# Performance work log

Measured on AMD Instinct MI355X. Metric: run time of the kernel, lower is better.

Reference implementation:

```python
import jax, jax.numpy as jnp
import numpy as np

B, N, D_IN, D_OUT = 8, 2048, 64, 64


def setup_inputs() -> dict:
    key = jax.random.key(0)
    k1, k2, k3, k4 = jax.random.split(key, 4)
    x = jax.random.normal(k1, (B, N, D_IN), dtype=jnp.float32)
    adj_matrix = jax.random.randint(k2, (B, N, N), 0, 2, dtype=jnp.int32)
    W = jax.random.normal(k3, (D_IN, D_OUT), dtype=jnp.float32) * (1.0 / np.sqrt(D_IN))
    a = jax.random.normal(k4, (2 * D_OUT,), dtype=jnp.float32) * (1.0 / np.sqrt(2 * D_OUT))
    return {"x": x, "adj_matrix": adj_matrix, "W": W, "a": a}


def reference(x, adj_matrix, W, a):
    # h = W(x): [B, N, D_OUT]
    h = jnp.einsum('bnd,de->bne', x, W)
    d_out = W.shape[1]
    # a([h_i || h_j]) == h_i @ a_src + h_j @ a_dst  (same math, no O(N^2*2D) concat)
    a_src, a_dst = a[:d_out], a[d_out:]
    e_src = h @ a_src  # [B, N]
    e_dst = h @ a_dst  # [B, N]
    e = e_src[:, :, None] + e_dst[:, None, :]  # [B, N, N]
    e = jax.nn.leaky_relu(e, negative_slope=0.2)
    e = jnp.where(adj_matrix == 0, jnp.float32(-1e9), e)
    alpha = jax.nn.softmax(e, axis=-1)  # [B, N, N]
    # dropout is identity in eval mode
    h_prime = jnp.einsum('bnm,bmd->bnd', alpha, h)
    return h_prime
```

## Files before the change

kernel.cpp:

```cpp
#include <hip/hip_runtime.h>

typedef unsigned short u16;
typedef unsigned int u32;
using short8 = __attribute__((ext_vector_type(8))) short;
using half8  = __attribute__((ext_vector_type(8))) _Float16;
using f32x4  = __attribute__((ext_vector_type(4))) float;

#define NB 8
#define NN 2048

#define EDL_OFF   0
#define RSL_OFF   4096
#define DBUF_OFF  4608
#define ROWB      144
#define SLAB_SZ   9216
#define BUFSTRIDE 18432
#define SMEM_SZ   41472

__device__ __forceinline__ u16 f2h(float f) {
    _Float16 h = (_Float16)f;
    union { _Float16 h; u16 u; } cvt; cvt.h = h;
    return cvt.u;
}

__global__ __launch_bounds__(256, 2) void gat_k1(
    const float* __restrict__ x, const float* __restrict__ W, const float* __restrict__ a,
    u16* __restrict__ hT,
    float* __restrict__ es, float* __restrict__ ed)
{
    const int tid  = threadIdx.x;
    const int lane = tid & 63;
    const int wid  = tid >> 6;
    const int rowbase = blockIdx.x * 16;
    const int b    = rowbase >> 11;
    const int col0 = rowbase & 2047;

    __shared__ float xs[16][64];
    __shared__ u16 lh[64][20];

    {
        const float4 v = *reinterpret_cast<const float4*>(x + (size_t)rowbase * 64 + tid * 4);
        *reinterpret_cast<float4*>(&xs[0][0] + tid * 4) = v;
    }

    float Wc[64];
#pragma unroll
    for (int k = 0; k < 64; ++k) Wc[k] = W[k * 64 + lane];
    const float asrc = a[lane], adst = a[64 + lane];
    __syncthreads();

#pragma unroll
    for (int r = 0; r < 4; ++r) {
        const int row = wid * 4 + r;
        float acc = 0.f;
#pragma unroll
        for (int kq = 0; kq < 16; ++kq) {
            const float4 xv = *reinterpret_cast<const float4*>(&xs[row][kq * 4]);
            acc = fmaf(xv.x, Wc[kq * 4 + 0], acc);
            acc = fmaf(xv.y, Wc[kq * 4 + 1], acc);
            acc = fmaf(xv.z, Wc[kq * 4 + 2], acc);
            acc = fmaf(xv.w, Wc[kq * 4 + 3], acc);
        }
        float vs = acc * asrc, vd = acc * adst;
#pragma unroll
        for (int off = 32; off; off >>= 1) {
            vs += __shfl_xor(vs, off, 64);
            vd += __shfl_xor(vd, off, 64);
        }
        if (lane == 0) { es[rowbase + row] = vs; ed[rowbase + row] = vd; }
        lh[lane][row] = f2h(acc);
    }
    __syncthreads();

    {
        const int d = tid >> 2, part = tid & 3;
        u32 h0 = lh[d][part*4+0] | ((u32)lh[d][part*4+1] << 16);
        u32 h1 = lh[d][part*4+2] | ((u32)lh[d][part*4+3] << 16);
        size_t goff = (size_t)(b * 64 + d) * 2048 + col0 + part * 4;
        *reinterpret_cast<uint2*>(hT + goff) = make_uint2(h0, h1);
    }
}

#define SM_HALF(EOFF, AA, AB, PA)                                                 \
{                                                                                 \
    const float4 e0 = *reinterpret_cast<const float4*>(edq + (EOFF));             \
    const float4 e1 = *reinterpret_cast<const float4*>(edq + (EOFF) + 4);         \
    const float ev[8] = {e0.x,e0.y,e0.z,e0.w,e1.x,e1.y,e1.z,e1.w};                \
    const int av[8] = {AA.x,AA.y,AA.z,AA.w,AB.x,AB.y,AB.z,AB.w};                  \
    float pe[8];                                                                  \
    _Pragma("unroll")                                                             \
    for (int q = 0; q < 8; ++q) {                                                 \
        const float tt = es_i + ev[q];                                            \
        const float eL = fmaxf(tt, 0.2f * tt);                                    \
        const float p  = __builtin_amdgcn_exp2f(eL * L2E);                        \
        pe[q] = av[q] ? p : 0.f;                                                  \
    }                                                                             \
    rs += ((pe[0]+pe[1]) + (pe[2]+pe[3])) + ((pe[4]+pe[5]) + (pe[6]+pe[7]));      \
    _Pragma("unroll")                                                             \
    for (int q = 0; q < 8; ++q) PA[q] = (_Float16)pe[q];                          \
}

#define WIN_STEP(WIN, A0, A1, A2, A3)                                             \
{                                                                                 \
    const int wo = (WIN) * 64;                                                    \
    short8 nh0 = {}, nh1 = {};                                                    \
    if ((WIN) < 7) {         \
        nh0 = *reinterpret_cast<const short8*>(hT + gb + wo + 64);                \
        nh1 = *reinterpret_cast<const short8*>(hT + gb + wo + 72);                \
    }                                                                             \
    half8 pa0, pa1;                                                               \
    SM_HALF(wo,      A0, A1, pa0)                                                 \
    SM_HALF(wo + 32, A2, A3, pa1)                                                 \
    if ((WIN) < 6) {          \
        A0 = *reinterpret_cast<const int4*>(arow + wo + 128);                     \
        A1 = *reinterpret_cast<const int4*>(arow + wo + 132);                     \
        A2 = *reinterpret_cast<const int4*>(arow + wo + 160);                     \
        A3 = *reinterpret_cast<const int4*>(arow + wo + 164);                     \
    }                                                                             \
    const char* slab = ((WIN) & 1) ? slabB : slabA;                               \
    half8 f0 = *reinterpret_cast<const half8*>(slab + fo);                        \
    half8 f1 = *reinterpret_cast<const half8*>(slab + 2304 + fo);                 \
    half8 f2 = *reinterpret_cast<const half8*>(slab + 4608 + fo);                 \
    half8 f3 = *reinterpret_cast<const half8*>(slab + 6912 + fo);                 \
    half8 g0 = *reinterpret_cast<const half8*>(slab + 64 + fo);                   \
    half8 g1 = *reinterpret_cast<const half8*>(slab + 64 + 2304 + fo);            \
    half8 g2 = *reinterpret_cast<const half8*>(slab + 64 + 4608 + fo);            \
    half8 g3 = *reinterpret_cast<const half8*>(slab + 64 + 6912 + fo);            \
    acc0 = __builtin_amdgcn_mfma_f32_16x16x32_f16(pa0, f0, acc0, 0, 0, 0);        \
    acc1 = __builtin_amdgcn_mfma_f32_16x16x32_f16(pa0, f1, acc1, 0, 0, 0);        \
    acc2 = __builtin_amdgcn_mfma_f32_16x16x32_f16(pa0, f2, acc2, 0, 0, 0);        \
    acc3 = __builtin_amdgcn_mfma_f32_16x16x32_f16(pa0, f3, acc3, 0, 0, 0);        \
    acc0 = __builtin_amdgcn_mfma_f32_16x16x32_f16(pa1, g0, acc0, 0, 0, 0);        \
    acc1 = __builtin_amdgcn_mfma_f32_16x16x32_f16(pa1, g1, acc1, 0, 0, 0);        \
    acc2 = __builtin_amdgcn_mfma_f32_16x16x32_f16(pa1, g2, acc2, 0, 0, 0);        \
    acc3 = __builtin_amdgcn_mfma_f32_16x16x32_f16(pa1, g3, acc3, 0, 0, 0);        \
    if ((WIN) < 7) {                                                              \
        char* nslab = ((WIN) & 1) ? slabA : slabB;                                \
        *reinterpret_cast<short8*>(nslab + swoff)      = nh0;                     \
        *reinterpret_cast<short8*>(nslab + swoff + 16) = nh1;                     \
    }                                                                             \
    __syncthreads();                                                              \
}

__global__ __launch_bounds__(512, 2) void gat_k3(
    const int* __restrict__ adj,
    const u16* __restrict__ hT,
    const float* __restrict__ es, const float* __restrict__ ed,
    float* __restrict__ acc_part, float* __restrict__ rs_part)
{
    __shared__ char smem[SMEM_SZ] __attribute__((aligned(16)));
    const int g = blockIdx.x;
    const int b     = g & 7;
    const int t2    = g >> 3;
    const int itile = t2 & 31;
    const int jhalf = t2 >> 5;
    const int tid  = threadIdx.x;
    const int lane = tid & 63;
    const int w    = tid >> 6;
    const int rg   = w & 3;
    const int jq   = w >> 2;
    const int li   = lane & 15;
    const int lg   = lane >> 4;
    const int cb   = jhalf * 1024;
    const int gr0  = b * 2048 + itile * 64;

    {
        float* edL = (float*)(smem + EDL_OFF);
        edL[tid]       = ed[b * 2048 + cb + tid];
        edL[tid + 512] = ed[b * 2048 + cb + tid + 512];
    }
    const float es_i = es[gr0 + rg * 16 + li];
    const float L2E  = 1.44269504088896f;

    const int* __restrict__ arow =
        adj + (size_t)(gr0 + rg * 16 + li) * 2048 + cb + jq * 512 + lg * 8;

    const int dd  = rg * 16 + (lane >> 2);
    const size_t gb = (size_t)(b * 64 + dd) * 2048 + cb + jq * 512 + (lane & 3) * 16;
    const int swoff = dd * ROWB + (lane & 3) * 32;

    char* slabA = smem + DBUF_OFF + jq * SLAB_SZ;
    char* slabB = slabA + BUFSTRIDE;

    int4 pA0 = *reinterpret_cast<const int4*>(arow);
    int4 pA1 = *reinterpret_cast<const int4*>(arow + 4);
    int4 pA2 = *reinterpret_cast<const int4*>(arow + 32);
    int4 pA3 = *reinterpret_cast<const int4*>(arow + 36);
    int4 pB0 = *reinterpret_cast<const int4*>(arow + 64);
    int4 pB1 = *reinterpret_cast<const int4*>(arow + 68);
    int4 pB2 = *reinterpret_cast<const int4*>(arow + 96);
    int4 pB3 = *reinterpret_cast<const int4*>(arow + 100);
    {
        short8 h0 = *reinterpret_cast<const short8*>(hT + gb);
        short8 h1 = *reinterpret_cast<const short8*>(hT + gb + 8);
        *reinterpret_cast<short8*>(slabA + swoff)      = h0;
        *reinterpret_cast<short8*>(slabA + swoff + 16) = h1;
    }
    __syncthreads();

    f32x4 acc0 = {0.f,0.f,0.f,0.f}, acc1 = {0.f,0.f,0.f,0.f};
    f32x4 acc2 = {0.f,0.f,0.f,0.f}, acc3 = {0.f,0.f,0.f,0.f};
    float rs = 0.f;
    const float* edq = (const float*)(smem + EDL_OFF) + jq * 512 + lg * 8;
    const int fo = li * ROWB + lg * 16;

    WIN_STEP(0, pA0, pA1, pA2, pA3)
    WIN_STEP(1, pB0, pB1, pB2, pB3)
    WIN_STEP(2, pA0, pA1, pA2, pA3)
    WIN_STEP(3, pB0, pB1, pB2, pB3)
    WIN_STEP(4, pA0, pA1, pA2, pA3)
    WIN_STEP(5, pB0, pB1, pB2, pB3)
    WIN_STEP(6, pA0, pA1, pA2, pA3)
    WIN_STEP(7, pB0, pB1, pB2, pB3)

    rs += __shfl_xor(rs, 16, 64);
    rs += __shfl_xor(rs, 32, 64);
    float* rsL = (float*)(smem + RSL_OFF);
    if (lane < 16) rsL[jq * 64 + rg * 16 + li] = rs;

    float* accL = (float*)(smem + DBUF_OFF);
    {
        f32x4 accs[4] = {acc0, acc1, acc2, acc3};
#pragma unroll
        for (int dt = 0; dt < 4; ++dt)
#pragma unroll
            for (int r = 0; r < 4; ++r)
                accL[(w * 16 + 4 * lg + r) * 64 + dt * 16 + li] = accs[dt][r];
    }
    __syncthreads();

    {
#pragma unroll
        for (int rep = 0; rep < 2; ++rep) {
            const int fi = (rep * 512 + tid) * 4;
            const int r  = fi >> 6;
            const int d0 = fi & 63;
            const int rgo = r >> 4, ri = r & 15;
            const float4 u0 = *reinterpret_cast<const float4*>(accL + ((0 + rgo) * 16 + ri) * 64 + d0);
            const float4 u1 = *reinterpret_cast<const float4*>(accL + ((4 + rgo) * 16 + ri) * 64 + d0);
            float4 o = make_float4(u0.x+u1.x, u0.y+u1.y, u0.z+u1.z, u0.w+u1.w);
            *reinterpret_cast<float4*>(acc_part + ((size_t)jhalf * 16384 + gr0 + r) * 64 + d0) = o;
        }
        if (tid < 64)
            rs_part[(size_t)jhalf * 16384 + gr0 + tid] = rsL[tid] + rsL[64 + tid];
    }
}

__global__ __launch_bounds__(512) void gat_k4(
    const float4* __restrict__ ap, const float* __restrict__ rp,
    float4* __restrict__ out)
{
    const int idx = blockIdx.x * 512 + threadIdx.x;
    const int row = idx >> 4;
    const float4 u0 = ap[idx];
    const float4 u1 = ap[262144 + idx];
    const float inv = 1.0f / (rp[row] + rp[16384 + row]);
    out[idx] = make_float4((u0.x+u1.x)*inv, (u0.y+u1.y)*inv,
                           (u0.z+u1.z)*inv, (u0.w+u1.w)*inv);
}

extern "C" void kernel_launch(void* const* d_in, const int* in_sizes, int n_in,
                              void* d_out, int out_size, void* d_ws, size_t ws_size,
                              hipStream_t stream)
{
    const float* x   = (const float*)d_in[0];
    const int*   adj = (const int*)d_in[1];
    const float* W   = (const float*)d_in[2];
    const float* a   = (const float*)d_in[3];
    float* out = (float*)d_out;

    char* ws = (char*)d_ws;
    size_t off = 0;
    auto carve = [&](size_t bytes) -> void* {
        void* p = ws + off;
        off += (bytes + 255) & ~(size_t)255;
        return p;
    };
    u16*   hT       = (u16*)  carve((size_t)NB * 64 * NN * 2);
    float* es       = (float*)carve((size_t)NB * NN * 4);
    float* ed       = (float*)carve((size_t)NB * NN * 4);
    float* acc_part = (float*)carve((size_t)2 * NB * NN * 64 * 4);
    float* rs_part  = (float*)carve((size_t)2 * NB * NN * 4);
    (void)ws_size; (void)in_sizes; (void)n_in; (void)out_size;

    gat_k1<<<NB * NN / 16, 256, 0, stream>>>(x, W, a, hT, es, ed);
    gat_k3<<<2 * NB * NN / 64, 512, 0, stream>>>(adj, hT, es, ed, acc_part, rs_part);
    gat_k4<<<512, 512, 0, stream>>>((const float4*)acc_part, rs_part, (float4*)out);
}
```

Measured before the change: 40.17 us.

## Drop split-K over columns and fuse final normalization into attention kernel

```diff
diff --git a/kernel.cpp b/kernel.cpp
--- a/kernel.cpp
+++ b/kernel.cpp
@@ -10,12 +10,12 @@
 #define NN 2048
 
 #define EDL_OFF   0
-#define RSL_OFF   4096
-#define DBUF_OFF  4608
+#define DBUF_OFF  8192
 #define ROWB      144
 #define SLAB_SZ   9216
-#define BUFSTRIDE 18432
-#define SMEM_SZ   41472
+#define BUFSTRIDE 36864
+#define RSL_OFF   (DBUF_OFF + 32768)
+#define SMEM_SZ   81920
 
 __device__ __forceinline__ u16 f2h(float f) {
     _Float16 h = (_Float16)f;
@@ -103,15 +103,17 @@
 #define WIN_STEP(WIN, A0, A1, A2, A3)                                             \
 {                                                                                 \
     const int wo = (WIN) * 64;                                                    \
-    short8 nh0 = {}, nh1 = {};                                                    \
-    if ((WIN) < 7) {         \
+    short8 nh0 = {}, nh1 = {}, nh2 = {}, nh3 = {};                                \
+    if ((WIN) < 7) {                                                              \
         nh0 = *reinterpret_cast<const short8*>(hT + gb + wo + 64);                \
         nh1 = *reinterpret_cast<const short8*>(hT + gb + wo + 72);                \
+        nh2 = *reinterpret_cast<const short8*>(hT + gb + wo + 80);                \
+        nh3 = *reinterpret_cast<const short8*>(hT + gb + wo + 88);                \
     }                                                                             \
     half8 pa0, pa1;                                                               \
     SM_HALF(wo,      A0, A1, pa0)                                                 \
     SM_HALF(wo + 32, A2, A3, pa1)                                                 \
-    if ((WIN) < 6) {          \
+    if ((WIN) < 6) {                                                              \
         A0 = *reinterpret_cast<const int4*>(arow + wo + 128);                     \
         A1 = *reinterpret_cast<const int4*>(arow + wo + 132);                     \
         A2 = *reinterpret_cast<const int4*>(arow + wo + 160);                     \
@@ -138,46 +140,47 @@
         char* nslab = ((WIN) & 1) ? slabA : slabB;                                \
         *reinterpret_cast<short8*>(nslab + swoff)      = nh0;                     \
         *reinterpret_cast<short8*>(nslab + swoff + 16) = nh1;                     \
+        *reinterpret_cast<short8*>(nslab + swoff + 32) = nh2;                     \
+        *reinterpret_cast<short8*>(nslab + swoff + 48) = nh3;                     \
     }                                                                             \
     __syncthreads();                                                              \
 }
 
-__global__ __launch_bounds__(512, 2) void gat_k3(
+__global__ __launch_bounds__(512, 4) void gat_k3(
     const int* __restrict__ adj,
     const u16* __restrict__ hT,
     const float* __restrict__ es, const float* __restrict__ ed,
-    float* __restrict__ acc_part, float* __restrict__ rs_part)
+    float* __restrict__ out)
 {
     __shared__ char smem[SMEM_SZ] __attribute__((aligned(16)));
     const int g = blockIdx.x;
     const int b     = g & 7;
-    const int t2    = g >> 3;
-    const int itile = t2 & 31;
-    const int jhalf = t2 >> 5;
+    const int itile = g >> 3;
     const int tid  = threadIdx.x;
     const int lane = tid & 63;
     const int w    = tid >> 6;
-    const int rg   = w & 3;
-    const int jq   = w >> 2;
+    const int rg   = w >> 2;
+    const int jq   = w & 3;
     const int li   = lane & 15;
     const int lg   = lane >> 4;
-    const int cb   = jhalf * 1024;
-    const int gr0  = b * 2048 + itile * 64;
+    const int gr0  = b * 2048 + itile * 32;
 
     {
         float* edL = (float*)(smem + EDL_OFF);
-        edL[tid]       = ed[b * 2048 + cb + tid];
-        edL[tid + 512] = ed[b * 2048 + cb + tid + 512];
+#pragma unroll
+        for (int rep = 0; rep < 4; ++rep)
+            edL[rep * 512 + tid] = ed[b * 2048 + rep * 512 + tid];
     }
     const float es_i = es[gr0 + rg * 16 + li];
     const float L2E  = 1.44269504088896f;
 
     const int* __restrict__ arow =
-        adj + (size_t)(gr0 + rg * 16 + li) * 2048 + cb + jq * 512 + lg * 8;
-
-    const int dd  = rg * 16 + (lane >> 2);
-    const size_t gb = (size_t)(b * 64 + dd) * 2048 + cb + jq * 512 + (lane & 3) * 16;
-    const int swoff = dd * ROWB + (lane & 3) * 32;
+        adj + (size_t)(gr0 + rg * 16 + li) * 2048 + jq * 512 + lg * 8;
+
+    const int dd  = rg * 32 + (lane >> 1);
+    const int jp  = lane & 1;
+    const size_t gb = (size_t)(b * 64 + dd) * 2048 + jq * 512 + jp * 32;
+    const int swoff = dd * ROWB + jp * 64;
 
     char* slabA = smem + DBUF_OFF + jq * SLAB_SZ;
     char* slabB = slabA + BUFSTRIDE;
@@ -193,8 +196,12 @@
     {
         short8 h0 = *reinterpret_cast<const short8*>(hT + gb);
         short8 h1 = *reinterpret_cast<const short8*>(hT + gb + 8);
+        short8 h2 = *reinterpret_cast<const short8*>(hT + gb + 16);
+        short8 h3 = *reinterpret_cast<const short8*>(hT + gb + 24);
         *reinterpret_cast<short8*>(slabA + swoff)      = h0;
         *reinterpret_cast<short8*>(slabA + swoff + 16) = h1;
+        *reinterpret_cast<short8*>(slabA + swoff + 32) = h2;
+        *reinterpret_cast<short8*>(slabA + swoff + 48) = h3;
     }
     __syncthreads();
 
@@ -215,10 +222,9 @@
 
     rs += __shfl_xor(rs, 16, 64);
     rs += __shfl_xor(rs, 32, 64);
-    float* rsL = (float*)(smem + RSL_OFF);
-    if (lane < 16) rsL[jq * 64 + rg * 16 + li] = rs;
-
+    float* rsL  = (float*)(smem + RSL_OFF);
     float* accL = (float*)(smem + DBUF_OFF);
+    if (lane < 16) rsL[jq * 32 + rg * 16 + li] = rs;
     {
         f32x4 accs[4] = {acc0, acc1, acc2, acc3};
 #pragma unroll
@@ -230,33 +236,24 @@
     __syncthreads();
 
     {
-#pragma unroll
-        for (int rep = 0; rep < 2; ++rep) {
-            const int fi = (rep * 512 + tid) * 4;
-            const int r  = fi >> 6;
-            const int d0 = fi & 63;
-            const int rgo = r >> 4, ri = r & 15;
-            const float4 u0 = *reinterpret_cast<const float4*>(accL + ((0 + rgo) * 16 + ri) * 64 + d0);
-            const float4 u1 = *reinterpret_cast<const float4*>(accL + ((4 + rgo) * 16 + ri) * 64 + d0);
-            float4 o = make_float4(u0.x+u1.x, u0.y+u1.y, u0.z+u1.z, u0.w+u1.w);
-            *reinterpret_cast<float4*>(acc_part + ((size_t)jhalf * 16384 + gr0 + r) * 64 + d0) = o;
+        const int r  = tid >> 4;
+        const int d0 = (tid & 15) * 4;
+        const int rgo = r >> 4, ri = r & 15;
+        const float s = (rsL[0 * 32 + r] + rsL[1 * 32 + r])
+                      + (rsL[2 * 32 + r] + rsL[3 * 32 + r]);
+        const float inv = 1.0f / s;
+        float4 o;
+        float* o4 = &o.x;
+#pragma unroll
+        for (int e = 0; e < 4; ++e) {
+            float v = 0.f;
+#pragma unroll
+            for (int cc = 0; cc < 4; ++cc)
+                v += accL[((rgo * 4 + cc) * 16 + ri) * 64 + d0 + e];
+            o4[e] = v * inv;
         }
-        if (tid < 64)
-            rs_part[(size_t)jhalf * 16384 + gr0 + tid] = rsL[tid] + rsL[64 + tid];
-    }
-}
-
-__global__ __launch_bounds__(512) void gat_k4(
-    const float4* __restrict__ ap, const float* __restrict__ rp,
-    float4* __restrict__ out)
-{
-    const int idx = blockIdx.x * 512 + threadIdx.x;
-    const int row = idx >> 4;
-    const float4 u0 = ap[idx];
-    const float4 u1 = ap[262144 + idx];
-    const float inv = 1.0f / (rp[row] + rp[16384 + row]);
-    out[idx] = make_float4((u0.x+u1.x)*inv, (u0.y+u1.y)*inv,
-                           (u0.z+u1.z)*inv, (u0.w+u1.w)*inv);
+        *reinterpret_cast<float4*>(out + ((size_t)(gr0 + r) * 64 + d0)) = o;
+    }
 }
 
 extern "C" void kernel_launch(void* const* d_in, const int* in_sizes, int n_in,
@@ -276,14 +273,11 @@
         off += (bytes + 255) & ~(size_t)255;
         return p;
     };
-    u16*   hT       = (u16*)  carve((size_t)NB * 64 * NN * 2);
-    float* es       = (float*)carve((size_t)NB * NN * 4);
-    float* ed       = (float*)carve((size_t)NB * NN * 4);
-    float* acc_part = (float*)carve((size_t)2 * NB * NN * 64 * 4);
-    float* rs_part  = (float*)carve((size_t)2 * NB * NN * 4);
+    u16*   hT = (u16*)  carve((size_t)NB * 64 * NN * 2);
+    float* es = (float*)carve((size_t)NB * NN * 4);
+    float* ed = (float*)carve((size_t)NB * NN * 4);
     (void)ws_size; (void)in_sizes; (void)n_in; (void)out_size;
 
     gat_k1<<<NB * NN / 16, 256, 0, stream>>>(x, W, a, hT, es, ed);
-    gat_k3<<<2 * NB * NN / 64, 512, 0, stream>>>(adj, hT, es, ed, acc_part, rs_part);
-    gat_k4<<<512, 512, 0, stream>>>((const float4*)acc_part, rs_part, (float4*)out);
-}
+    gat_k3<<<NB * NN / 32, 512, 0, stream>>>(adj, hT, es, ed, out);
+}
```

Measured after the change: 39.95 us. Within noise of the previous version (-0.5%).
